# Kernel tuning notes

Measured on AMD Instinct MI355X. Metric: run time of the kernel, lower is better.

Reference implementation:

```python
import jax, jax.numpy as jnp
import numpy as np

WS, SS, P, H = 7, 3, 14, 12  # window, shift, patch grid, heads
NW = (P // WS) ** 2          # windows per image = 4
N_WIN = WS * WS              # tokens per window = 49

def _rel_pos_index():
    coords = np.stack(np.meshgrid(np.arange(WS), np.arange(WS), indexing='ij')).reshape(2, -1)
    rel = (coords[:, :, None] - coords[:, None, :]).transpose(1, 2, 0).astype(np.int64)
    rel[..., 0] += WS - 1
    rel[..., 1] += WS - 1
    rel[..., 0] *= 2 * WS - 1
    return rel.sum(-1)  # [49,49]

def _shift_mask():
    img = np.zeros((P, P))
    sl = (slice(0, -WS), slice(-WS, -SS), slice(-SS, None))
    cnt = 0
    for h in sl:
        for w in sl:
            img[h, w] = cnt
            cnt += 1
    mw = img.reshape(P // WS, WS, P // WS, WS).transpose(0, 2, 1, 3).reshape(-1, N_WIN)
    am = mw[:, None, :] - mw[:, :, None]
    return np.where(am != 0, -100.0, 0.0).astype(np.float32)  # [nW,49,49]

RPI = jnp.asarray(_rel_pos_index())
MASK = jnp.asarray(_shift_mask())

def _hswish(x):
    return x * jnp.clip(x + 3.0, 0.0, 6.0) / 6.0

def _hsig(x):
    return jnp.clip(x + 3.0, 0.0, 6.0) / 6.0

def _bn(x, g, b, eps=1e-5):
    # training-mode batchnorm over (B,H,W) per channel, biased variance
    m = x.mean((0, 2, 3), keepdims=True)
    v = ((x - m) ** 2).mean((0, 2, 3), keepdims=True)
    return (x - m) / jnp.sqrt(v + eps) * g[None, :, None, None] + b[None, :, None, None]

def setup_inputs() -> dict:
    key = jax.random.key(0)
    ks = jax.random.split(key, 20)
    C, HID = 768, 3072
    return {
        'x': jax.random.normal(ks[0], (32, 197, C), jnp.float32),
        'w_qkv': jax.random.normal(ks[1], (3 * C, C), jnp.float32) * 0.02,
        'w_proj': jax.random.normal(ks[2], (C, C), jnp.float32) * 0.02,
        'b_proj': jax.random.normal(ks[3], (C,), jnp.float32) * 0.02,
        'rpb_table': jax.random.normal(ks[4], ((2 * WS - 1) ** 2, H), jnp.float32) * 0.02,
        'pw1_w': jax.random.normal(ks[5], (HID, C), jnp.float32) * 0.02,
        'bn1_g': 1.0 + jax.random.normal(ks[6], (HID,), jnp.float32) * 0.02,
        'bn1_b': jax.random.normal(ks[7], (HID,), jnp.float32) * 0.02,
        'dw_w': jax.random.normal(ks[8], (HID, 3, 3), jnp.float32) * 0.1,
        'bn2_g': 1.0 + jax.random.normal(ks[9], (HID,), jnp.float32) * 0.02,
        'bn2_b': jax.random.normal(ks[10], (HID,), jnp.float32) * 0.02,
        'se_w1': jax.random.normal(ks[11], (HID // 4, HID), jnp.float32) * 0.02,
        'se_b1': jax.random.normal(ks[12], (HID // 4,), jnp.float32) * 0.02,
        'se_w2': jax.random.normal(ks[13], (HID, HID // 4), jnp.float32) * 0.02,
        'se_b2': jax.random.normal(ks[14], (HID,), jnp.float32) * 0.02,
        'pw2_w': jax.random.normal(ks[15], (C, HID), jnp.float32) * 0.02,
        'bn3_g': 1.0 + jax.random.normal(ks[16], (C,), jnp.float32) * 0.02,
        'bn3_b': jax.random.normal(ks[17], (C,), jnp.float32) * 0.02,
    }

def reference(x, w_qkv, w_proj, b_proj, rpb_table, pw1_w, bn1_g, bn1_b, dw_w,
              bn2_g, bn2_b, se_w1, se_b1, se_w2, se_b2, pw2_w, bn3_g, bn3_b):
    B, N, C = x.shape
    hd = C // H
    scale = hd ** -0.5
    nw = P // WS

    cls_tok = x[:, :1]
    xs = x[:, 1:].reshape(B, P, P, C)
    xs = jnp.roll(xs, (-SS, -SS), axis=(1, 2))  # cyclic shift
    # window partition -> [B*nW, 49, C]
    win = xs.reshape(B, nw, WS, nw, WS, C).transpose(0, 1, 3, 2, 4, 5).reshape(B * NW, N_WIN, C)

    qkv = (win @ w_qkv.T).reshape(B * NW, N_WIN, 3, H, hd).transpose(2, 0, 3, 1, 4)
    q, k, v = qkv[0], qkv[1], qkv[2]  # [B*nW, H, 49, hd]
    attn = jnp.einsum('bhqd,bhkd->bhqk', q, k) * scale
    # relative position bias gather: [H,49,49]
    bias = rpb_table[RPI.reshape(-1)].reshape(N_WIN, N_WIN, H).transpose(2, 0, 1)
    attn = attn + bias[None]
    # shifted-window mask add
    attn = (attn.reshape(B, NW, H, N_WIN, N_WIN) + MASK[None, :, None]).reshape(B * NW, H, N_WIN, N_WIN)
    attn = jax.nn.softmax(attn, axis=-1)
    out = jnp.einsum('bhqk,bhkd->bhqd', attn, v).transpose(0, 2, 1, 3).reshape(B * NW, N_WIN, C)
    out = out @ w_proj.T + b_proj

    # window reverse + reverse shift
    xs = out.reshape(B, nw, nw, WS, WS, C).transpose(0, 1, 3, 2, 4, 5).reshape(B, P, P, C)
    xs = jnp.roll(xs, (SS, SS), axis=(1, 2))
    x = jnp.concatenate([cls_tok, xs.reshape(B, P * P, C)], axis=1)

    # LocalityFeedForward (inverted residual conv MLP with SE)
    cls_tok, xt = x[:, :1], x[:, 1:]
    f = xt.transpose(0, 2, 1).reshape(B, C, P, P)
    h = _hswish(_bn(jnp.einsum('bchw,oc->bohw', f, pw1_w), bn1_g, bn1_b))
    h = _hswish(_bn(jax.lax.conv_general_dilated(
        h, dw_w[:, None], (1, 1), 'SAME',
        feature_group_count=h.shape[1],
        dimension_numbers=('NCHW', 'OIHW', 'NCHW')), bn2_g, bn2_b))
    s = h.mean((2, 3))  # global avg pool [B, hid]
    s = _hsig(jax.nn.relu(s @ se_w1.T + se_b1) @ se_w2.T + se_b2)
    h = h * s[:, :, None, None]
    h = _bn(jnp.einsum('bchw,oc->bohw', h, pw2_w), bn3_g, bn3_b)
    f = f + h
    x = jnp.concatenate([cls_tok, f.reshape(B, C, P * P).transpose(0, 2, 1)], axis=1)
    return x
```

## Files before the change

### kernel.cpp

```cpp
#include <hip/hip_runtime.h>
#include <hip/hip_bf16.h>

typedef unsigned short ushort_t;
typedef unsigned int uint_t;
typedef short short8 __attribute__((ext_vector_type(8)));
typedef float floatx4 __attribute__((ext_vector_type(4)));

__device__ inline float b2f(ushort_t u){
    uint_t v = ((uint_t)u) << 16;
    return __uint_as_float(v);
}
__device__ inline ushort_t f2b(float f){
    uint_t v = __float_as_uint(f);
    uint_t r = (v + 0x7FFFu + ((v >> 16) & 1u)) >> 16;
    return (ushort_t)r;
}
__device__ inline void unpack8(uint4 u, float* f){
    uint_t w[4] = {u.x, u.y, u.z, u.w};
    #pragma unroll
    for (int i = 0; i < 4; ++i){
        f[2*i]   = __uint_as_float(w[i] << 16);
        f[2*i+1] = __uint_as_float(w[i] & 0xFFFF0000u);
    }
}
__device__ inline uint4 pack8(const float* f){
    uint4 o;
    uint_t w[4];
    #pragma unroll
    for (int i = 0; i < 4; ++i)
        w[i] = (uint_t)f2b(f[2*i]) | ((uint_t)f2b(f[2*i+1]) << 16);
    o.x = w[0]; o.y = w[1]; o.z = w[2]; o.w = w[3];
    return o;
}
__device__ inline ushort4 cvt4(float4 v){
    ushort4 o;
    o.x = f2b(v.x); o.y = f2b(v.y); o.z = f2b(v.z); o.w = f2b(v.w);
    return o;
}
__device__ inline float hswish(float y){
    return y * fminf(fmaxf(y + 3.f, 0.f), 6.f) * (1.f/6.f);
}

#define MROWS 6272
#define CDIM  768
#define HID   3072
#define QKV3  2304

__device__ inline int scatter_row(int ri){
    int w  = ri / 49, t = ri % 49;
    int b  = w >> 2,  wi = w & 3;
    int wy = wi >> 1, wx = wi & 1;
    int ty = t / 7,   tx = t % 7;
    int yd = (wy*7 + ty + 3) % 14;
    int xd = (wx*7 + tx + 3) % 14;
    return b*196 + yd*14 + xd;
}

__global__ __launch_bounds__(256) void cvt_f2b(const float4* __restrict__ in,
                                               ushort4* __restrict__ out, int n4){
    int i = blockIdx.x * 256 + threadIdx.x;
    if (i < n4) out[i] = cvt4(in[i]);
}

__global__ __launch_bounds__(256) void dw_transpose(const float* __restrict__ w,
                                                    float* __restrict__ wT){
    int i = blockIdx.x*256 + threadIdx.x;
    if (i < HID*9){ int c = i/9, k = i%9; wT[k*HID + c] = w[i]; }
}

__global__ __launch_bounds__(256) void gather_win(const float4* __restrict__ x,
                                                  ushort4* __restrict__ win){
    int idx = blockIdx.x * 256 + threadIdx.x;
    if (idx >= MROWS * 192) return;
    int r  = idx / 192, c4 = idx % 192;
    int w  = r / 49,  t  = r % 49;
    int b  = w >> 2,  wi = w & 3;
    int wy = wi >> 1, wx = wi & 1;
    int ty = t / 7,   tx = t % 7;
    int ys = (wy*7 + ty + 3) % 14;
    int xs = (wx*7 + tx + 3) % 14;
    win[idx] = cvt4(x[(size_t)b*197*192 + (size_t)(1 + ys*14 + xs)*192 + c4]);
}

__global__ __launch_bounds__(256) void gemm_bt(const ushort_t* __restrict__ A,
                                               const ushort_t* __restrict__ B,
                                               ushort_t* __restrict__ Cb,
                                               float* __restrict__ Cf,
                                               int M, int N, int K,
                                               const float* __restrict__ bias,
                                               float* __restrict__ stats,
                                               int scat){
    const int nx   = gridDim.x;
    int flat = blockIdx.y * nx + blockIdx.x;
    int xcd  = flat & 7;
    int k    = flat >> 3;
    int by   = xcd + 8 * (k / nx);
    int bx   = k % nx;
    if (by * 128 >= M) return;

    __shared__ __align__(16) ushort_t As[2][128*32];
    __shared__ __align__(16) ushort_t Bs[2][128*32];
    const int tid  = threadIdx.x;
    const int lane = tid & 63;
    const int wid  = tid >> 6;
    const int m0 = by * 128;
    const int n0 = bx * 128;
    const int wm = (wid >> 1) * 64;
    const int wn = (wid & 1) * 64;

    const int srow = (lane >> 2);
    const int scol = (((lane & 3) ^ ((lane >> 3) & 3)) * 8);

    floatx4 acc[4][4] = {};

    auto stage = [&](int buf, int k0){
        #pragma unroll
        for (int j = 0; j < 2; ++j){
            int ch  = wid*2 + j;
            const ushort_t* gA = A + (size_t)(m0 + ch*16 + srow)*K + k0 + scol;
            const ushort_t* gB = B + (size_t)(n0 + ch*16 + srow)*K + k0 + scol;
            __builtin_amdgcn_global_load_lds(
                (const __attribute__((address_space(1))) void*)gA,
                (__attribute__((address_space(3))) void*)(&As[buf][ch*512 + lane*8]), 16, 0, 0);
            __builtin_amdgcn_global_load_lds(
                (const __attribute__((address_space(1))) void*)gB,
                (__attribute__((address_space(3))) void*)(&Bs[buf][ch*512 + lane*8]), 16, 0, 0);
        }
    };

    const int NK = K >> 5;
    stage(0, 0);

    const int fr   = lane & 15;
    const int quad = lane >> 4;
    const int cosw = (quad ^ ((fr >> 1) & 3)) * 8;
    int cur = 0;
    for (int it = 0; it < NK; ++it){
        __builtin_amdgcn_sched_barrier(0);
        __builtin_amdgcn_s_barrier();
        if (it + 1 < NK){
            stage(cur ^ 1, (it + 1) << 5);
            asm volatile("s_waitcnt vmcnt(4)" ::: "memory");
        } else {
            asm volatile("s_waitcnt vmcnt(0)" ::: "memory");
        }
        __builtin_amdgcn_s_barrier();
        __builtin_amdgcn_sched_barrier(0);

        short8 af[4], bfr[4];
        #pragma unroll
        for (int i = 0; i < 4; ++i){
            af[i]  = *(const short8*)(&As[cur][(wm + i*16 + fr)*32 + cosw]);
            bfr[i] = *(const short8*)(&Bs[cur][(wn + i*16 + fr)*32 + cosw]);
        }
        #pragma unroll
        for (int i = 0; i < 4; ++i)
            #pragma unroll
            for (int j = 0; j < 4; ++j)
                acc[i][j] = __builtin_amdgcn_mfma_f32_16x16x32_bf16(af[i], bfr[j], acc[i][j], 0, 0, 0);
        cur ^= 1;
    }

    #pragma unroll
    for (int i = 0; i < 4; ++i){
        int grow = m0 + wm + i*16 + (lane >> 4)*4;
        #pragma unroll
        for (int j = 0; j < 4; ++j){
            int gcol = n0 + wn + j*16 + (lane & 15);
            float bv = bias ? bias[gcol] : 0.f;
            if (scat){
                #pragma unroll
                for (int r = 0; r < 4; ++r){
                    float v = acc[i][j][r] + bv;
                    size_t off = (size_t)scatter_row(grow + r)*N + gcol;
                    Cf[off] = v;
                    Cb[off] = f2b(v);
                }
            } else if (Cb){
                #pragma unroll
                for (int r = 0; r < 4; ++r)
                    Cb[(size_t)(grow + r)*N + gcol] = f2b(acc[i][j][r] + bv);
            } else {
                #pragma unroll
                for (int r = 0; r < 4; ++r)
                    Cf[(size_t)(grow + r)*N + gcol] = acc[i][j][r] + bv;
            }
        }
    }

    if (stats){
        #pragma unroll
        for (int j = 0; j < 4; ++j){
            int gcol = n0 + wn + j*16 + (lane & 15);
            float bv = bias ? bias[gcol] : 0.f;
            float sv = 0.f, sq = 0.f;
            #pragma unroll
            for (int i = 0; i < 4; ++i)
                #pragma unroll
                for (int r = 0; r < 4; ++r){
                    float v = acc[i][j][r] + bv;
                    sv += v; sq += v*v;
                }
            sv += __shfl_xor(sv, 16, 64);  sq += __shfl_xor(sq, 16, 64);
            sv += __shfl_xor(sv, 32, 64);  sq += __shfl_xor(sq, 32, 64);
            if (lane < 16){
                atomicAdd(&stats[gcol], sv);
                atomicAdd(&stats[N + gcol], sq);
            }
        }
    }
}

__global__ __launch_bounds__(256) void gemm_bt64(const ushort_t* __restrict__ A,
                                                 const ushort_t* __restrict__ B,
                                                 ushort_t* __restrict__ Cb,
                                                 float* __restrict__ Cf,
                                                 int M, int N, int K,
                                                 const float* __restrict__ bias,
                                                 float* __restrict__ stats,
                                                 int scat){
    const int nx   = gridDim.x;
    int flat = blockIdx.y * nx + blockIdx.x;
    int xcd  = flat & 7;
    int k    = flat >> 3;
    int by   = xcd + 8 * (k / nx);
    int bx   = k % nx;
    if (by * 128 >= M) return;

    __shared__ __align__(16) ushort_t As[2][128*32];
    __shared__ __align__(16) ushort_t Bs[2][64*32];
    const int tid  = threadIdx.x;
    const int lane = tid & 63;
    const int wid  = tid >> 6;
    const int m0 = by * 128;
    const int n0 = bx * 64;
    const int wm = (wid >> 1) * 64;
    const int wn = (wid & 1) * 32;

    const int srow = (lane >> 2);
    const int scol = (((lane & 3) ^ ((lane >> 3) & 3)) * 8);

    floatx4 acc[4][2] = {};

    auto stage = [&](int buf, int k0){
        #pragma unroll
        for (int j = 0; j < 2; ++j){
            int ch = wid*2 + j;
            const ushort_t* gA = A + (size_t)(m0 + ch*16 + srow)*K + k0 + scol;
            __builtin_amdgcn_global_load_lds(
                (const __attribute__((address_space(1))) void*)gA,
                (__attribute__((address_space(3))) void*)(&As[buf][ch*512 + lane*8]), 16, 0, 0);
        }
        const ushort_t* gB = B + (size_t)(n0 + wid*16 + srow)*K + k0 + scol;
        __builtin_amdgcn_global_load_lds(
            (const __attribute__((address_space(1))) void*)gB,
            (__attribute__((address_space(3))) void*)(&Bs[buf][wid*512 + lane*8]), 16, 0, 0);
    };

    const int NK = K >> 5;
    stage(0, 0);

    const int fr   = lane & 15;
    const int quad = lane >> 4;
    const int cosw = (quad ^ ((fr >> 1) & 3)) * 8;
    int cur = 0;
    for (int it = 0; it < NK; ++it){
        __builtin_amdgcn_sched_barrier(0);
        __builtin_amdgcn_s_barrier();
        if (it + 1 < NK){
            stage(cur ^ 1, (it + 1) << 5);
            asm volatile("s_waitcnt vmcnt(3)" ::: "memory");
        } else {
            asm volatile("s_waitcnt vmcnt(0)" ::: "memory");
        }
        __builtin_amdgcn_s_barrier();
        __builtin_amdgcn_sched_barrier(0);

        short8 af[4], bfr[2];
        #pragma unroll
        for (int i = 0; i < 4; ++i)
            af[i]  = *(const short8*)(&As[cur][(wm + i*16 + fr)*32 + cosw]);
        #pragma unroll
        for (int j = 0; j < 2; ++j)
            bfr[j] = *(const short8*)(&Bs[cur][(wn + j*16 + fr)*32 + cosw]);
        #pragma unroll
        for (int i = 0; i < 4; ++i)
            #pragma unroll
            for (int j = 0; j < 2; ++j)
                acc[i][j] = __builtin_amdgcn_mfma_f32_16x16x32_bf16(af[i], bfr[j], acc[i][j], 0, 0, 0);
        cur ^= 1;
    }

    #pragma unroll
    for (int i = 0; i < 4; ++i){
        int grow = m0 + wm + i*16 + (lane >> 4)*4;
        #pragma unroll
        for (int j = 0; j < 2; ++j){
            int gcol = n0 + wn + j*16 + (lane & 15);
            float bv = bias ? bias[gcol] : 0.f;
            if (scat){
                #pragma unroll
                for (int r = 0; r < 4; ++r){
                    float v = acc[i][j][r] + bv;
                    size_t off = (size_t)scatter_row(grow + r)*N + gcol;
                    Cf[off] = v;
                    Cb[off] = f2b(v);
                }
            } else if (Cb){
                #pragma unroll
                for (int r = 0; r < 4; ++r)
                    Cb[(size_t)(grow + r)*N + gcol] = f2b(acc[i][j][r] + bv);
            } else {
                #pragma unroll
                for (int r = 0; r < 4; ++r)
                    Cf[(size_t)(grow + r)*N + gcol] = acc[i][j][r] + bv;
            }
        }
    }

    if (stats){
        #pragma unroll
        for (int j = 0; j < 2; ++j){
            int gcol = n0 + wn + j*16 + (lane & 15);
            float bv = bias ? bias[gcol] : 0.f;
            float sv = 0.f, sq = 0.f;
            #pragma unroll
            for (int i = 0; i < 4; ++i)
                #pragma unroll
                for (int r = 0; r < 4; ++r){
                    float v = acc[i][j][r] + bv;
                    sv += v; sq += v*v;
                }
            sv += __shfl_xor(sv, 16, 64);  sq += __shfl_xor(sq, 16, 64);
            sv += __shfl_xor(sv, 32, 64);  sq += __shfl_xor(sq, 32, 64);
            if (lane < 16){
                atomicAdd(&stats[gcol], sv);
                atomicAdd(&stats[N + gcol], sq);
            }
        }
    }
}

__global__ __launch_bounds__(256) void bm_precompute(const float* __restrict__ rpb,
                                                     float* __restrict__ bm){
    int idx = blockIdx.x*256 + threadIdx.x;
    if (idx >= 12*4*64*64) return;
    int ki = idx & 63, qi = (idx >> 6) & 63, wi = (idx >> 12) & 3, h = idx >> 14;
    float v = -1e30f;
    if (qi < 49 && ki < 49){
        int qy = qi/7, qx = qi%7, ky = ki/7, kx = ki%7;
        int ridx = (qy - ky + 6)*13 + (qx - kx + 6);
        v = rpb[ridx*12 + h];
        int wy = wi >> 1, wx = wi & 1;
        int gqy = wy*7 + qy, gqx = wx*7 + qx, gky = wy*7 + ky, gkx = wx*7 + kx;
        int cq = ((gqy < 7) ? 0 : (gqy < 11 ? 1 : 2))*3 + ((gqx < 7) ? 0 : (gqx < 11 ? 1 : 2));
        int ck = ((gky < 7) ? 0 : (gky < 11 ? 1 : 2))*3 + ((gkx < 7) ? 0 : (gkx < 11 ? 1 : 2));
        if (cq != ck) v -= 100.f;
    }
    bm[idx] = v;
}

__global__ __launch_bounds__(256) void attn_mfma(const ushort_t* __restrict__ qkv,
                                                 ushort_t* __restrict__ outp,
                                                 const float* __restrict__ bm){
    __shared__ __align__(16) ushort_t Ps[64*72];
    __shared__ __align__(16) ushort_t VT[64*72];
    const int tid = threadIdx.x, lane = tid & 63, wid = tid >> 6;
    const int h = blockIdx.x, w = blockIdx.y, wi = w & 3;
    const int fr = lane & 15, quad = lane >> 4, co = quad*8;

    for (int idx = tid; idx < 64*64; idx += 256){
        int k = idx >> 6, n = idx & 63;
        ushort_t v = 0;
        if (k < 49) v = qkv[(size_t)(w*49 + k)*QKV3 + 1536 + h*64 + n];
        VT[n*72 + k] = v;
    }
    __syncthreads();

    floatx4 accs[4] = {};
    const ushort_t* qbase = qkv + (size_t)(w*49 + wid*16 + fr)*QKV3 + h*64;
    #pragma unroll
    for (int k0 = 0; k0 < 64; k0 += 32){
        short8 af = *(const short8*)(qbase + k0 + co);
        #pragma unroll
        for (int j = 0; j < 4; ++j){
            const ushort_t* kbase = qkv + (size_t)(w*49 + j*16 + fr)*QKV3 + 768 + h*64;
            short8 bf = *(const short8*)(kbase + k0 + co);
            accs[j] = __builtin_amdgcn_mfma_f32_16x16x32_bf16(af, bf, accs[j], 0, 0, 0);
        }
    }

    const float* bmh = bm + (size_t)((h*4 + wi)*64 + wid*16)*64;
    #pragma unroll
    for (int r = 0; r < 4; ++r){
        int lrow = quad*4 + r;
        float m = -3e38f;
        #pragma unroll
        for (int j = 0; j < 4; ++j){
            float a = accs[j][r]*0.125f + bmh[lrow*64 + j*16 + fr];
            accs[j][r] = a;
            m = fmaxf(m, a);
        }
        #pragma unroll
        for (int off = 1; off < 16; off <<= 1) m = fmaxf(m, __shfl_xor(m, off, 64));
        float s = 0.f;
        #pragma unroll
        for (int j = 0; j < 4; ++j){
            float e = __expf(accs[j][r] - m);
            accs[j][r] = e; s += e;
        }
        #pragma unroll
        for (int off = 1; off < 16; off <<= 1) s += __shfl_xor(s, off, 64);
        float inv = 1.f / s;
        #pragma unroll
        for (int j = 0; j < 4; ++j)
            Ps[(wid*16 + lrow)*72 + j*16 + fr] = f2b(accs[j][r]*inv);
    }
    __syncthreads();

    floatx4 acco[4] = {};
    #pragma unroll
    for (int k0 = 0; k0 < 64; k0 += 32){
        short8 af = *(const short8*)(Ps + (wid*16 + fr)*72 + k0 + co);
        #pragma unroll
        for (int j = 0; j < 4; ++j){
            short8 bf = *(const short8*)(VT + (j*16 + fr)*72 + k0 + co);
            acco[j] = __builtin_amdgcn_mfma_f32_16x16x32_bf16(af, bf, acco[j], 0, 0, 0);
        }
    }
    #pragma unroll
    for (int r = 0; r < 4; ++r){
        int qi = wid*16 + quad*4 + r;
        if (qi < 49){
            #pragma unroll
            for (int j = 0; j < 4; ++j)
                outp[(size_t)(w*49 + qi)*CDIM + h*64 + j*16 + fr] = f2b(acco[j][r]);
        }
    }
}

__global__ void zero_f32(float* __restrict__ p, int n){
    int i = blockIdx.x*256 + threadIdx.x;
    if (i < n) p[i] = 0.f;
}
__global__ __launch_bounds__(256) void bn_stats_v(const ushort_t* __restrict__ X,
                                                  float* __restrict__ sums){
    const int cgl = threadIdx.x & 31;
    const int rp  = threadIdx.x >> 5;
    const int cg  = blockIdx.x*32 + cgl;
    const int r0  = blockIdx.y*224;
    const uint4* Xb = (const uint4*)X;
    float s[8] = {}, q[8] = {};
    for (int r = r0 + rp; r < r0 + 224; r += 8){
        uint4 u = Xb[(size_t)r*384 + cg];
        float f[8]; unpack8(u, f);
        #pragma unroll
        for (int e = 0; e < 8; ++e){ s[e] += f[e]; q[e] += f[e]*f[e]; }
    }
    #pragma unroll
    for (int e = 0; e < 8; ++e){
        s[e] += __shfl_xor(s[e], 32, 64);
        q[e] += __shfl_xor(q[e], 32, 64);
    }
    __shared__ float red[4][32][17];
    const int wv = threadIdx.x >> 6;
    if ((threadIdx.x & 32) == 0){
        #pragma unroll
        for (int e = 0; e < 8; ++e){
            red[wv][cgl][e]   = s[e];
            red[wv][cgl][8+e] = q[e];
        }
    }
    __syncthreads();
    #pragma unroll
    for (int k = 0; k < 2; ++k){
        int o = threadIdx.x*2 + k;
        int cgo = o >> 4, e = o & 15;
        float v = red[0][cgo][e] + red[1][cgo][e] + red[2][cgo][e] + red[3][cgo][e];
        int c = blockIdx.x*256 + cgo*8 + (e & 7);
        atomicAdd(&sums[(e < 8 ? 0 : HID) + c], v);
    }
}
__global__ void bn_finalize(float* __restrict__ sums, const float* __restrict__ g,
                            const float* __restrict__ b, int Cch){
    int c = blockIdx.x*256 + threadIdx.x;
    if (c >= Cch) return;
    float mean = sums[c] * (1.f/6272.f);
    float var  = sums[Cch + c] * (1.f/6272.f) - mean*mean;
    float sc = g[c] * rsqrtf(var + 1e-5f);
    sums[c] = sc;
    sums[Cch + c] = b[c] - mean*sc;
}

__global__ __launch_bounds__(256) void dwconv_v(const ushort_t* __restrict__ in,
                                                const float* __restrict__ wT,
                                                const float* __restrict__ ss,
                                                ushort_t* __restrict__ out){
    int idx = blockIdx.x*256 + threadIdx.x;
    if (idx >= MROWS*384) return;
    int r  = idx / 384, cg = idx % 384;
    int b  = r / 196,  p  = r % 196;
    int y  = p / 14,   x  = p % 14;
    int c  = cg*8;
    const uint4* inb = (const uint4*)(in + (size_t)b*196*HID);
    float sc[8], sh[8];
    {
        const float4* s0 = (const float4*)(ss + c);
        const float4* s1 = (const float4*)(ss + HID + c);
        float4 a0 = s0[0], a1 = s0[1], b0 = s1[0], b1 = s1[1];
        sc[0]=a0.x; sc[1]=a0.y; sc[2]=a0.z; sc[3]=a0.w;
        sc[4]=a1.x; sc[5]=a1.y; sc[6]=a1.z; sc[7]=a1.w;
        sh[0]=b0.x; sh[1]=b0.y; sh[2]=b0.z; sh[3]=b0.w;
        sh[4]=b1.x; sh[5]=b1.y; sh[6]=b1.z; sh[7]=b1.w;
    }
    float acc[8] = {};
    #pragma unroll
    for (int ky = 0; ky < 3; ++ky){
        int yy = y + ky - 1;
        if ((unsigned)yy >= 14u) continue;
        #pragma unroll
        for (int kx = 0; kx < 3; ++kx){
            int xx = x + kx - 1;
            if ((unsigned)xx >= 14u) continue;
            uint4 u = inb[(yy*14 + xx)*384 + cg];
            float fin[8]; unpack8(u, fin);
            const float4* wp = (const float4*)(wT + (ky*3 + kx)*HID + c);
            float4 w0 = wp[0], w1 = wp[1];
            float wv[8] = {w0.x,w0.y,w0.z,w0.w,w1.x,w1.y,w1.z,w1.w};
            #pragma unroll
            for (int e = 0; e < 8; ++e)
                acc[e] += hswish(fin[e]*sc[e] + sh[e]) * wv[e];
        }
    }
    ((uint4*)out)[idx] = pack8(acc);
}

__global__ __launch_bounds__(256) void se_mean_v(const ushort_t* __restrict__ X,
                                                 const float* __restrict__ ss,
                                                 float* __restrict__ s){
    const int b   = blockIdx.x;
    const int cgl = threadIdx.x & 31;
    const int rp  = threadIdx.x >> 5;
    const int cg  = blockIdx.y*32 + cgl;
    const int c   = cg*8;
    float sc[8], sh[8];
    #pragma unroll
    for (int e = 0; e < 8; ++e){ sc[e] = ss[c+e]; sh[e] = ss[HID+c+e]; }
    const uint4* Xb = (const uint4*)(X + (size_t)b*196*HID);
    float a[8] = {};
    for (int p = rp; p < 196; p += 8){
        uint4 u = Xb[(size_t)p*384 + cg];
        float f[8]; unpack8(u, f);
        #pragma unroll
        for (int e = 0; e < 8; ++e) a[e] += hswish(f[e]*sc[e] + sh[e]);
    }
    #pragma unroll
    for (int e = 0; e < 8; ++e) a[e] += __shfl_xor(a[e], 32, 64);
    __shared__ float red[4][32][9];
    const int wv = threadIdx.x >> 6;
    if ((threadIdx.x & 32) == 0){
        #pragma unroll
        for (int e = 0; e < 8; ++e) red[wv][cgl][e] = a[e];
    }
    __syncthreads();
    {
        int o = threadIdx.x;
        int cgo = o >> 3, e = o & 7;
        float v = red[0][cgo][e] + red[1][cgo][e] + red[2][cgo][e] + red[3][cgo][e];
        s[(size_t)b*HID + blockIdx.y*256 + cgo*8 + e] = v * (1.f/196.f);
    }
}
__global__ __launch_bounds__(256) void se_fc(const float* __restrict__ in,
                                             const float* __restrict__ w,
                                             const float* __restrict__ bias,
                                             float* __restrict__ out,
                                             int IN, int OUT, int mode){
    int wv   = (blockIdx.x*256 + threadIdx.x) >> 6;
    int lane = threadIdx.x & 63;
    if (wv >= OUT) return;
    const float* wr = w + (size_t)wv * IN;
    float acc[32];
    #pragma unroll
    for (int b = 0; b < 32; ++b) acc[b] = 0.f;
    for (int k = lane; k < IN; k += 64){
        float wval = wr[k];
        #pragma unroll
        for (int b = 0; b < 32; ++b)
            acc[b] += in[b*IN + k] * wval;
    }
    #pragma unroll
    for (int b = 0; b < 32; ++b){
        float v = acc[b];
        #pragma unroll
        for (int off = 32; off; off >>= 1) v += __shfl_down(v, off, 64);
        if (lane == 0){
            float a = v + bias[wv];
            if (mode == 0) a = fmaxf(a, 0.f);
            else           a = fminf(fmaxf(a + 3.f, 0.f), 6.f) * (1.f/6.f);
            out[b*OUT + wv] = a;
        }
    }
}
__global__ __launch_bounds__(256) void se_scale(ushort_t* __restrict__ X,
                                                const float* __restrict__ ss,
                                                const float* __restrict__ s2){
    int idx = blockIdx.x*256 + threadIdx.x;
    if (idx >= MROWS * (HID/8)) return;
    int r = idx / (HID/8), c8 = idx % (HID/8);
    int b = r / 196;
    int c = c8*8;
    uint4 u = ((uint4*)X)[idx];
    float f[8]; unpack8(u, f);
    const float* sp = s2 + b*HID + c;
    #pragma unroll
    for (int e = 0; e < 8; ++e)
        f[e] = hswish(f[e]*ss[c+e] + ss[HID+c+e]) * sp[e];
    ((uint4*)X)[idx] = pack8(f);
}

__global__ __launch_bounds__(256) void final_k(const float4* __restrict__ xin,
                                               const float4* __restrict__ f,
                                               const float4* __restrict__ h4,
                                               const float* __restrict__ ss,
                                               float4* __restrict__ outp){
    int idx = blockIdx.x*256 + threadIdx.x;
    if (idx >= 32*197*192) return;
    int b = idx / (197*192);
    int rem = idx % (197*192);
    int n = rem / 192, c4 = rem % 192;
    if (n == 0){ outp[idx] = xin[idx]; return; }
    size_t off = ((size_t)b*196 + n - 1)*192 + c4;
    float4 hv = h4[off];
    float4 fv = f[off];
    float4 o;
    int c = c4*4;
    o.x = fv.x + hv.x*ss[c+0] + ss[CDIM + c+0];
    o.y = fv.y + hv.y*ss[c+1] + ss[CDIM + c+1];
    o.z = fv.z + hv.z*ss[c+2] + ss[CDIM + c+2];
    o.w = fv.w + hv.w*ss[c+3] + ss[CDIM + c+3];
    outp[idx] = o;
}

extern "C" void kernel_launch(void* const* d_in, const int* in_sizes, int n_in,
                              void* d_out, int out_size, void* d_ws, size_t ws_size,
                              hipStream_t stream){
    const float* x      = (const float*)d_in[0];
    const float* w_qkv  = (const float*)d_in[1];
    const float* w_proj = (const float*)d_in[2];
    const float* b_proj = (const float*)d_in[3];
    const float* rpb    = (const float*)d_in[4];
    const float* pw1_w  = (const float*)d_in[5];
    const float* bn1_g  = (const float*)d_in[6];
    const float* bn1_b  = (const float*)d_in[7];
    const float* dw_w   = (const float*)d_in[8];
    const float* bn2_g  = (const float*)d_in[9];
    const float* bn2_b  = (const float*)d_in[10];
    const float* se_w1  = (const float*)d_in[11];
    const float* se_b1  = (const float*)d_in[12];
    const float* se_w2  = (const float*)d_in[13];
    const float* se_b2  = (const float*)d_in[14];
    const float* pw2_w  = (const float*)d_in[15];
    const float* bn3_g  = (const float*)d_in[16];
    const float* bn3_b  = (const float*)d_in[17];

    char* ws = (char*)d_ws;
    ushort_t* win    = (ushort_t*)(ws + 0);
    float*    bm     = (float*)(ws + 0);
    ushort_t* qkv    = (ushort_t*)(ws + 9633792);
    ushort_t* fbf    = (ushort_t*)(ws + 0);
    ushort_t* pw1b   = (ushort_t*)(ws + 9633792);
    ushort_t* hb     = (ushort_t*)(ws + 0);
    ushort_t* wqkvb  = (ushort_t*)(ws + 38535168);
    ushort_t* attnb  = (ushort_t*)(ws + 38535168);
    ushort_t* wprojb = (ushort_t*)(ws + 48168960);
    ushort_t* ha     = (ushort_t*)(ws + 38535168);
    float*    h4     = (float*)(ws + 38535168);
    ushort_t* pw2b   = (ushort_t*)(ws + 57802752);
    float*    f      = (float*)(ws + 77070336);
    float*    stats  = (float*)(ws + 96337920);
    float*    s      = (float*)(ws + 96362496);
    float*    s1     = (float*)(ws + 96755712);
    float*    s2     = (float*)(ws + 96854016);
    float*    dwwT   = (float*)(ws + 96854016);

    const int vec_rows = (MROWS*192 + 255)/256;
    const int vec_hid8 = (MROWS*(HID/8) + 255)/256;
    const int GY = 56;

    dw_transpose<<<(HID*9 + 255)/256, 256, 0, stream>>>(dw_w, dwwT);
    cvt_f2b<<<(QKV3*CDIM/4 + 255)/256, 256, 0, stream>>>((const float4*)w_qkv, (ushort4*)wqkvb, QKV3*CDIM/4);
    cvt_f2b<<<(CDIM*CDIM/4 + 255)/256, 256, 0, stream>>>((const float4*)w_proj, (ushort4*)wprojb, CDIM*CDIM/4);

    gather_win<<<vec_rows, 256, 0, stream>>>((const float4*)x, (ushort4*)win);
    gemm_bt<<<dim3(QKV3/128, GY), 256, 0, stream>>>(win, wqkvb, qkv, nullptr, MROWS, QKV3, CDIM, nullptr, nullptr, 0);
    bm_precompute<<<(12*4*64*64)/256, 256, 0, stream>>>(rpb, bm);
    attn_mfma<<<dim3(12, 128), 256, 0, stream>>>(qkv, attnb, bm);
    cvt_f2b<<<(HID*CDIM/4 + 255)/256, 256, 0, stream>>>((const float4*)pw1_w, (ushort4*)pw1b, HID*CDIM/4);
    zero_f32<<<24, 256, 0, stream>>>(stats, 2*HID);
    gemm_bt64<<<dim3(CDIM/64, GY), 256, 0, stream>>>(attnb, wprojb, fbf, f, MROWS, CDIM, CDIM, b_proj, nullptr, 1);

    gemm_bt<<<dim3(HID/128, GY), 256, 0, stream>>>(fbf, pw1b, ha, nullptr, MROWS, HID, CDIM, nullptr, stats, 0);
    bn_finalize<<<HID/256, 256, 0, stream>>>(stats, bn1_g, bn1_b, HID);

    dwconv_v<<<(MROWS*384 + 255)/256, 256, 0, stream>>>(ha, dwwT, stats, hb);
    cvt_f2b<<<(CDIM*HID/4 + 255)/256, 256, 0, stream>>>((const float4*)pw2_w, (ushort4*)pw2b, CDIM*HID/4);
    zero_f32<<<24, 256, 0, stream>>>(stats, 2*HID);
    bn_stats_v<<<dim3(12, 28), 256, 0, stream>>>(hb, stats);
    bn_finalize<<<HID/256, 256, 0, stream>>>(stats, bn2_g, bn2_b, HID);

    se_mean_v<<<dim3(32, 12), 256, 0, stream>>>(hb, stats, s);
    se_fc<<<dim3((CDIM*64)/256), 256, 0, stream>>>(s, se_w1, se_b1, s1, HID, CDIM, 0);
    se_fc<<<dim3((HID*64)/256), 256, 0, stream>>>(s1, se_w2, se_b2, s2, CDIM, HID, 1);
    se_scale<<<vec_hid8, 256, 0, stream>>>(hb, stats, s2);

    zero_f32<<<6, 256, 0, stream>>>(stats, 2*CDIM);
    gemm_bt64<<<dim3(CDIM/64, GY), 256, 0, stream>>>(hb, pw2b, nullptr, h4, MROWS, CDIM, HID, nullptr, stats, 0);
    bn_finalize<<<CDIM/256, 256, 0, stream>>>(stats, bn3_g, bn3_b, CDIM);
    final_k<<<(32*197*192 + 255)/256, 256, 0, stream>>>((const float4*)x, (const float4*)f, (const float4*)h4, stats, (float4*)d_out);
}
```

Before: 542.2 us.

## Replace GEMM kernels with 256x128 tile, 512-thread, BK=64 unified kernel

Replaces the two GEMM variants (128x128 and 128x64 tiles, 256 threads, K-step 32) with one kernel using 256x128 output tiles, 8 waves, and a 64-wide K step staged as two 32-wide halves. Row loads are clamped and stores and stats are guarded so the ragged M (6272 rows) works with 256-row tiles. The kernel also raises wave priority around the MFMA bursts. The aim is more data reuse per tile, fewer barriers per K, and one kernel for all four GEMMs. In exchange it needs twice the LDS per block and launches fewer blocks, so GPU occupancy and the tail of the grid may suffer, especially for the N=768 GEMMs.

```diff
diff --git a/kernel.cpp b/kernel.cpp
--- a/kernel.cpp
+++ b/kernel.cpp
@@ -82,7 +82,7 @@
     win[idx] = cvt4(x[(size_t)b*197*192 + (size_t)(1 + ys*14 + xs)*192 + c4]);
 }
 
-__global__ __launch_bounds__(256) void gemm_bt(const ushort_t* __restrict__ A,
+__global__ __launch_bounds__(512) void gemm256(const ushort_t* __restrict__ A,
                                                const ushort_t* __restrict__ B,
                                                ushort_t* __restrict__ Cb,
                                                float* __restrict__ Cf,
@@ -96,14 +96,14 @@
     int k    = flat >> 3;
     int by   = xcd + 8 * (k / nx);
     int bx   = k % nx;
-    if (by * 128 >= M) return;
-
-    __shared__ __align__(16) ushort_t As[2][128*32];
-    __shared__ __align__(16) ushort_t Bs[2][128*32];
+    if (by * 256 >= M) return;
+
+    __shared__ __align__(16) ushort_t As[2][2][256*32];
+    __shared__ __align__(16) ushort_t Bs[2][2][128*32];
     const int tid  = threadIdx.x;
     const int lane = tid & 63;
     const int wid  = tid >> 6;
-    const int m0 = by * 128;
+    const int m0 = by * 256;
     const int n0 = bx * 128;
     const int wm = (wid >> 1) * 64;
     const int wn = (wid & 1) * 64;
@@ -115,20 +115,25 @@
 
     auto stage = [&](int buf, int k0){
         #pragma unroll
-        for (int j = 0; j < 2; ++j){
-            int ch  = wid*2 + j;
-            const ushort_t* gA = A + (size_t)(m0 + ch*16 + srow)*K + k0 + scol;
-            const ushort_t* gB = B + (size_t)(n0 + ch*16 + srow)*K + k0 + scol;
-            __builtin_amdgcn_global_load_lds(
-                (const __attribute__((address_space(1))) void*)gA,
-                (__attribute__((address_space(3))) void*)(&As[buf][ch*512 + lane*8]), 16, 0, 0);
+        for (int h = 0; h < 2; ++h){
+            #pragma unroll
+            for (int j = 0; j < 2; ++j){
+                int ch  = wid*2 + j;
+                int row = m0 + ch*16 + srow;
+                if (row > M-1) row = M-1;
+                const ushort_t* gA = A + (size_t)row*K + k0 + h*32 + scol;
+                __builtin_amdgcn_global_load_lds(
+                    (const __attribute__((address_space(1))) void*)gA,
+                    (__attribute__((address_space(3))) void*)(&As[buf][h][ch*512 + lane*8]), 16, 0, 0);
+            }
+            const ushort_t* gB = B + (size_t)(n0 + wid*16 + srow)*K + k0 + h*32 + scol;
             __builtin_amdgcn_global_load_lds(
                 (const __attribute__((address_space(1))) void*)gB,
-                (__attribute__((address_space(3))) void*)(&Bs[buf][ch*512 + lane*8]), 16, 0, 0);
+                (__attribute__((address_space(3))) void*)(&Bs[buf][h][wid*512 + lane*8]), 16, 0, 0);
         }
     };
 
-    const int NK = K >> 5;
+    const int NK = K >> 6;
     stage(0, 0);
 
     const int fr   = lane & 15;
@@ -139,51 +144,60 @@
         __builtin_amdgcn_sched_barrier(0);
         __builtin_amdgcn_s_barrier();
         if (it + 1 < NK){
-            stage(cur ^ 1, (it + 1) << 5);
-            asm volatile("s_waitcnt vmcnt(4)" ::: "memory");
+            stage(cur ^ 1, (it + 1) << 6);
+            asm volatile("s_waitcnt vmcnt(6)" ::: "memory");
         } else {
             asm volatile("s_waitcnt vmcnt(0)" ::: "memory");
         }
         __builtin_amdgcn_s_barrier();
         __builtin_amdgcn_sched_barrier(0);
 
-        short8 af[4], bfr[4];
-        #pragma unroll
-        for (int i = 0; i < 4; ++i){
-            af[i]  = *(const short8*)(&As[cur][(wm + i*16 + fr)*32 + cosw]);
-            bfr[i] = *(const short8*)(&Bs[cur][(wn + i*16 + fr)*32 + cosw]);
-        }
-        #pragma unroll
-        for (int i = 0; i < 4; ++i)
+        #pragma unroll
+        for (int h = 0; h < 2; ++h){
+            short8 af[4], bfr[4];
             #pragma unroll
-            for (int j = 0; j < 4; ++j)
-                acc[i][j] = __builtin_amdgcn_mfma_f32_16x16x32_bf16(af[i], bfr[j], acc[i][j], 0, 0, 0);
+            for (int i = 0; i < 4; ++i){
+                af[i]  = *(const short8*)(&As[cur][h][(wm + i*16 + fr)*32 + cosw]);
+                bfr[i] = *(const short8*)(&Bs[cur][h][(wn + i*16 + fr)*32 + cosw]);
+            }
+            __builtin_amdgcn_s_setprio(1);
+            #pragma unroll
+            for (int i = 0; i < 4; ++i)
+                #pragma unroll
+                for (int j = 0; j < 4; ++j)
+                    acc[i][j] = __builtin_amdgcn_mfma_f32_16x16x32_bf16(af[i], bfr[j], acc[i][j], 0, 0, 0);
+            __builtin_amdgcn_s_setprio(0);
+        }
         cur ^= 1;
     }
 
     #pragma unroll
     for (int i = 0; i < 4; ++i){
-        int grow = m0 + wm + i*16 + (lane >> 4)*4;
+        int grow = m0 + wm + i*16 + quad*4;
         #pragma unroll
         for (int j = 0; j < 4; ++j){
-            int gcol = n0 + wn + j*16 + (lane & 15);
+            int gcol = n0 + wn + j*16 + fr;
             float bv = bias ? bias[gcol] : 0.f;
             if (scat){
                 #pragma unroll
                 for (int r = 0; r < 4; ++r){
-                    float v = acc[i][j][r] + bv;
-                    size_t off = (size_t)scatter_row(grow + r)*N + gcol;
-                    Cf[off] = v;
-                    Cb[off] = f2b(v);
+                    if (grow + r < M){
+                        float v = acc[i][j][r] + bv;
+                        size_t off = (size_t)scatter_row(grow + r)*N + gcol;
+                        Cf[off] = v;
+                        Cb[off] = f2b(v);
+                    }
                 }
             } else if (Cb){
                 #pragma unroll
                 for (int r = 0; r < 4; ++r)
-                    Cb[(size_t)(grow + r)*N + gcol] = f2b(acc[i][j][r] + bv);
+                    if (grow + r < M)
+                        Cb[(size_t)(grow + r)*N + gcol] = f2b(acc[i][j][r] + bv);
             } else {
                 #pragma unroll
                 for (int r = 0; r < 4; ++r)
-                    Cf[(size_t)(grow + r)*N + gcol] = acc[i][j][r] + bv;
+                    if (grow + r < M)
+                        Cf[(size_t)(grow + r)*N + gcol] = acc[i][j][r] + bv;
             }
         }
     }
@@ -191,146 +205,20 @@
     if (stats){
         #pragma unroll
         for (int j = 0; j < 4; ++j){
-            int gcol = n0 + wn + j*16 + (lane & 15);
+            int gcol = n0 + wn + j*16 + fr;
             float bv = bias ? bias[gcol] : 0.f;
             float sv = 0.f, sq = 0.f;
             #pragma unroll
-            for (int i = 0; i < 4; ++i)
+            for (int i = 0; i < 4; ++i){
+                int grow = m0 + wm + i*16 + quad*4;
                 #pragma unroll
                 for (int r = 0; r < 4; ++r){
-                    float v = acc[i][j][r] + bv;
-                    sv += v; sq += v*v;
+                    if (grow + r < M){
+                        float v = acc[i][j][r] + bv;
+                        sv += v; sq += v*v;
+                    }
                 }
-            sv += __shfl_xor(sv, 16, 64);  sq += __shfl_xor(sq, 16, 64);
-            sv += __shfl_xor(sv, 32, 64);  sq += __shfl_xor(sq, 32, 64);
-            if (lane < 16){
-                atomicAdd(&stats[gcol], sv);
-                atomicAdd(&stats[N + gcol], sq);
             }
-        }
-    }
-}
-
-__global__ __launch_bounds__(256) void gemm_bt64(const ushort_t* __restrict__ A,
-                                                 const ushort_t* __restrict__ B,
-                                                 ushort_t* __restrict__ Cb,
-                                                 float* __restrict__ Cf,
-                                                 int M, int N, int K,
-                                                 const float* __restrict__ bias,
-                                                 float* __restrict__ stats,
-                                                 int scat){
-    const int nx   = gridDim.x;
-    int flat = blockIdx.y * nx + blockIdx.x;
-    int xcd  = flat & 7;
-    int k    = flat >> 3;
-    int by   = xcd + 8 * (k / nx);
-    int bx   = k % nx;
-    if (by * 128 >= M) return;
-
-    __shared__ __align__(16) ushort_t As[2][128*32];
-    __shared__ __align__(16) ushort_t Bs[2][64*32];
-    const int tid  = threadIdx.x;
-    const int lane = tid & 63;
-    const int wid  = tid >> 6;
-    const int m0 = by * 128;
-    const int n0 = bx * 64;
-    const int wm = (wid >> 1) * 64;
-    const int wn = (wid & 1) * 32;
-
-    const int srow = (lane >> 2);
-    const int scol = (((lane & 3) ^ ((lane >> 3) & 3)) * 8);
-
-    floatx4 acc[4][2] = {};
-
-    auto stage = [&](int buf, int k0){
-        #pragma unroll
-        for (int j = 0; j < 2; ++j){
-            int ch = wid*2 + j;
-            const ushort_t* gA = A + (size_t)(m0 + ch*16 + srow)*K + k0 + scol;
-            __builtin_amdgcn_global_load_lds(
-                (const __attribute__((address_space(1))) void*)gA,
-                (__attribute__((address_space(3))) void*)(&As[buf][ch*512 + lane*8]), 16, 0, 0);
-        }
-        const ushort_t* gB = B + (size_t)(n0 + wid*16 + srow)*K + k0 + scol;
-        __builtin_amdgcn_global_load_lds(
-            (const __attribute__((address_space(1))) void*)gB,
-            (__attribute__((address_space(3))) void*)(&Bs[buf][wid*512 + lane*8]), 16, 0, 0);
-    };
-
-    const int NK = K >> 5;
-    stage(0, 0);
-
-    const int fr   = lane & 15;
-    const int quad = lane >> 4;
-    const int cosw = (quad ^ ((fr >> 1) & 3)) * 8;
-    int cur = 0;
-    for (int it = 0; it < NK; ++it){
-        __builtin_amdgcn_sched_barrier(0);
-        __builtin_amdgcn_s_barrier();
-        if (it + 1 < NK){
-            stage(cur ^ 1, (it + 1) << 5);
-            asm volatile("s_waitcnt vmcnt(3)" ::: "memory");
-        } else {
-            asm volatile("s_waitcnt vmcnt(0)" ::: "memory");
-        }
-        __builtin_amdgcn_s_barrier();
-        __builtin_amdgcn_sched_barrier(0);
-
-        short8 af[4], bfr[2];
-        #pragma unroll
-        for (int i = 0; i < 4; ++i)
-            af[i]  = *(const short8*)(&As[cur][(wm + i*16 + fr)*32 + cosw]);
-        #pragma unroll
-        for (int j = 0; j < 2; ++j)
-            bfr[j] = *(const short8*)(&Bs[cur][(wn + j*16 + fr)*32 + cosw]);
-        #pragma unroll
-        for (int i = 0; i < 4; ++i)
-            #pragma unroll
-            for (int j = 0; j < 2; ++j)
-                acc[i][j] = __builtin_amdgcn_mfma_f32_16x16x32_bf16(af[i], bfr[j], acc[i][j], 0, 0, 0);
-        cur ^= 1;
-    }
-
-    #pragma unroll
-    for (int i = 0; i < 4; ++i){
-        int grow = m0 + wm + i*16 + (lane >> 4)*4;
-        #pragma unroll
-        for (int j = 0; j < 2; ++j){
-            int gcol = n0 + wn + j*16 + (lane & 15);
-            float bv = bias ? bias[gcol] : 0.f;
-            if (scat){
-                #pragma unroll
-                for (int r = 0; r < 4; ++r){
-                    float v = acc[i][j][r] + bv;
-                    size_t off = (size_t)scatter_row(grow + r)*N + gcol;
-                    Cf[off] = v;
-                    Cb[off] = f2b(v);
-                }
-            } else if (Cb){
-                #pragma unroll
-                for (int r = 0; r < 4; ++r)
-                    Cb[(size_t)(grow + r)*N + gcol] = f2b(acc[i][j][r] + bv);
-            } else {
-                #pragma unroll
-                for (int r = 0; r < 4; ++r)
-                    Cf[(size_t)(grow + r)*N + gcol] = acc[i][j][r] + bv;
-            }
-        }
-    }
-
-    if (stats){
-        #pragma unroll
-        for (int j = 0; j < 2; ++j){
-            int gcol = n0 + wn + j*16 + (lane & 15);
-            float bv = bias ? bias[gcol] : 0.f;
-            float sv = 0.f, sq = 0.f;
-            #pragma unroll
-            for (int i = 0; i < 4; ++i)
-                #pragma unroll
-                for (int r = 0; r < 4; ++r){
-                    float v = acc[i][j][r] + bv;
-                    sv += v; sq += v*v;
-                }
             sv += __shfl_xor(sv, 16, 64);  sq += __shfl_xor(sq, 16, 64);
             sv += __shfl_xor(sv, 32, 64);  sq += __shfl_xor(sq, 32, 64);
             if (lane < 16){
@@ -685,21 +573,21 @@
 
     const int vec_rows = (MROWS*192 + 255)/256;
     const int vec_hid8 = (MROWS*(HID/8) + 255)/256;
-    const int GY = 56;
+    const int GY = 32;
 
     dw_transpose<<<(HID*9 + 255)/256, 256, 0, stream>>>(dw_w, dwwT);
     cvt_f2b<<<(QKV3*CDIM/4 + 255)/256, 256, 0, stream>>>((const float4*)w_qkv, (ushort4*)wqkvb, QKV3*CDIM/4);
     cvt_f2b<<<(CDIM*CDIM/4 + 255)/256, 256, 0, stream>>>((const float4*)w_proj, (ushort4*)wprojb, CDIM*CDIM/4);
 
     gather_win<<<vec_rows, 256, 0, stream>>>((const float4*)x, (ushort4*)win);
-    gemm_bt<<<dim3(QKV3/128, GY), 256, 0, stream>>>(win, wqkvb, qkv, nullptr, MROWS, QKV3, CDIM, nullptr, nullptr, 0);
+    gemm256<<<dim3(QKV3/128, GY), 512, 0, stream>>>(win, wqkvb, qkv, nullptr, MROWS, QKV3, CDIM, nullptr, nullptr, 0);
     bm_precompute<<<(12*4*64*64)/256, 256, 0, stream>>>(rpb, bm);
     attn_mfma<<<dim3(12, 128), 256, 0, stream>>>(qkv, attnb, bm);
     cvt_f2b<<<(HID*CDIM/4 + 255)/256, 256, 0, stream>>>((const float4*)pw1_w, (ushort4*)pw1b, HID*CDIM/4);
     zero_f32<<<24, 256, 0, stream>>>(stats, 2*HID);
-    gemm_bt64<<<dim3(CDIM/64, GY), 256, 0, stream>>>(attnb, wprojb, fbf, f, MROWS, CDIM, CDIM, b_proj, nullptr, 1);
-
-    gemm_bt<<<dim3(HID/128, GY), 256, 0, stream>>>(fbf, pw1b, ha, nullptr, MROWS, HID, CDIM, nullptr, stats, 0);
+    gemm256<<<dim3(CDIM/128, GY), 512, 0, stream>>>(attnb, wprojb, fbf, f, MROWS, CDIM, CDIM, b_proj, nullptr, 1);
+
+    gemm256<<<dim3(HID/128, GY), 512, 0, stream>>>(fbf, pw1b, ha, nullptr, MROWS, HID, CDIM, nullptr, stats, 0);
     bn_finalize<<<HID/256, 256, 0, stream>>>(stats, bn1_g, bn1_b, HID);
 
     dwconv_v<<<(MROWS*384 + 255)/256, 256, 0, stream>>>(ha, dwwT, stats, hb);
@@ -714,7 +602,7 @@
     se_scale<<<vec_hid8, 256, 0, stream>>>(hb, stats, s2);
 
     zero_f32<<<6, 256, 0, stream>>>(stats, 2*CDIM);
-    gemm_bt64<<<dim3(CDIM/64, GY), 256, 0, stream>>>(hb, pw2b, nullptr, h4, MROWS, CDIM, HID, nullptr, stats, 0);
+    gemm256<<<dim3(CDIM/128, GY), 512, 0, stream>>>(hb, pw2b, nullptr, h4, MROWS, CDIM, HID, nullptr, stats, 0);
     bn_finalize<<<CDIM/256, 256, 0, stream>>>(stats, bn3_g, bn3_b, CDIM);
     final_k<<<(32*197*192 + 255)/256, 256, 0, stream>>>((const float4*)x, (const float4*)f, (const float4*)h4, stats, (float4*)d_out);
 }
```

After: 630.3 us. 1.16x slower.
